# Kernel optimization log

Measured on AMD Instinct MI355X. Metric: run time of the kernel, lower is better.

## Reference

```python
import jax, jax.numpy as jnp
import numpy as np

B, IN_UNITS, IN_CH, NUM_UNITS, UNIT_SIZE = 32, 16, 2048, 16, 64
NUM_ITERS = 2


def setup_inputs() -> dict:
    key = jax.random.key(0)
    k1, k2 = jax.random.split(key)
    x = jax.random.normal(k1, (B, IN_UNITS, IN_CH), dtype=jnp.float32)
    W = jax.random.normal(k2, (1, IN_CH, NUM_UNITS, UNIT_SIZE, IN_UNITS), dtype=jnp.float32)
    return {"x": x, "W": W}


def squash(s):
    # torch code sums squared magnitude over dim=2 (the num_units axis) with keepdim
    mag_sq = jnp.sum(s * s, axis=2, keepdims=True)
    mag = jnp.sqrt(mag_sq)
    return mag_sq / (1.0 + mag_sq) * (s / mag)


def reference(x, W):
    # x: (B, in_units, in_channels) -> (B, in_channels, in_units)
    xt = jnp.swapaxes(x, 1, 2)
    # u_hat[b,i,j,k] = sum_u W[0,i,j,k,u] * xt[b,i,u]  -> (B, IC, NU, US)
    u_hat = jnp.einsum('ijku,biu->bijk', W[0], xt)
    b_ij = jnp.zeros((1, IN_CH, NUM_UNITS, 1), dtype=x.dtype)
    v_j = None
    for _ in range(NUM_ITERS):
        # softmax over a singleton trailing dim -> all ones (faithful to source)
        c_ij = jax.nn.softmax(b_ij, axis=-1)  # (1, IC, NU, 1), broadcasts over batch
        s_j = jnp.sum(c_ij[None, ..., 0][0][None].squeeze(0) * 0 + c_ij * u_hat, axis=1, keepdims=True) if False else jnp.sum(c_ij * u_hat, axis=1, keepdims=True)  # (B,1,NU,US)
        v_j = squash(s_j)  # (B,1,NU,US)
        # agreement: <u_hat, v_j> over unit_size, broadcast v_j over in_channels
        u_vj1 = jnp.einsum('bijk,bljk->bij', u_hat, v_j)  # (B, IC, NU)
        u_vj1 = jnp.mean(u_vj1, axis=0, keepdims=True)[..., None]  # (1, IC, NU, 1)
        b_ij = b_ij + u_vj1
    return v_j[:, 0, :, :]  # (B, num_units, unit_size)
```

## Files before the change

### kernel.cpp

```cpp
#include <hip/hip_runtime.h>
#include <hip/hip_bf16.h>


#define B_SZ   32
#define IC     2048
#define NJ     16
#define NK     64
#define SOUT   (B_SZ*NJ*NK)
#define KSTEPS 1024
#define KSPLIT 32
#define SPW    (KSTEPS/KSPLIT)

typedef float v4f __attribute__((ext_vector_type(4)));
typedef short v8s __attribute__((ext_vector_type(8)));

static __device__ inline ushort f2bf(float f) {
    uint32_t u = __float_as_uint(f);
    u += 0x7FFFu + ((u >> 16) & 1u);
    return (ushort)(u >> 16);
}

__global__ __launch_bounds__(256)
void caps_xprep(const float* __restrict__ x, ushort* __restrict__ xb) {
    int gid  = blockIdx.x * 256 + threadIdx.x;
    int lane = gid & 63;
    int mt   = (gid >> 6) & 1;
    int step = gid >> 7;
    int q    = lane >> 4;
    int b    = mt * 16 + (lane & 15);
    int i    = 2 * step + (q >> 1);
    int u0   = (q & 1) * 8;

    const float* xp = x + (size_t)b * (16 * IC) + (size_t)u0 * IC + i;
    ushort tmp[8];
    #pragma unroll
    for (int jj = 0; jj < 8; ++jj)
        tmp[jj] = f2bf(xp[(size_t)jj * IC]);
    *(v8s*)(xb + (size_t)gid * 8) = *(const v8s*)tmp;
}

__global__ __launch_bounds__(256)
void caps_mfma(const ushort* __restrict__ xb, const float* __restrict__ W,
               float* __restrict__ part) {
    const int tid   = threadIdx.x;
    const int wv    = tid >> 6;
    const int lane  = tid & 63;
    const int j     = blockIdx.x;
    const int split = blockIdx.y;
    const int n     = lane & 15;
    const int q     = lane >> 4;
    const int step0 = split * SPW;

    v4f acc0 = {0.f, 0.f, 0.f, 0.f};
    v4f acc1 = {0.f, 0.f, 0.f, 0.f};

    const float*  wp = W + (size_t)(2 * step0 + (q >> 1)) * 16384
                         + (size_t)j * 1024 + (size_t)(wv * 16 + n) * 16 + (q & 1) * 8;
    const ushort* xp = xb + (size_t)step0 * 1024 + (size_t)lane * 8;

    #pragma unroll 4
    for (int s = 0; s < SPW; ++s) {
        float4 w0 = *(const float4*)(wp);
        float4 w1 = *(const float4*)(wp + 4);
        v8s a0 = *(const v8s*)(xp);
        v8s a1 = *(const v8s*)(xp + 512);
        v8s bb;
        bb[0] = (short)f2bf(w0.x); bb[1] = (short)f2bf(w0.y);
        bb[2] = (short)f2bf(w0.z); bb[3] = (short)f2bf(w0.w);
        bb[4] = (short)f2bf(w1.x); bb[5] = (short)f2bf(w1.y);
        bb[6] = (short)f2bf(w1.z); bb[7] = (short)f2bf(w1.w);
        acc0 = __builtin_amdgcn_mfma_f32_16x16x32_bf16(a0, bb, acc0, 0, 0, 0);
        acc1 = __builtin_amdgcn_mfma_f32_16x16x32_bf16(a1, bb, acc1, 0, 0, 0);
        wp += 2 * 16384;
        xp += 1024;
    }

    float* pp = part + (size_t)split * SOUT + (size_t)j * NK + wv * 16 + n;
    #pragma unroll
    for (int r = 0; r < 4; ++r) {
        int m = q * 4 + r;
        pp[(size_t)m * 1024]        = acc0[r];
        pp[(size_t)(m + 16) * 1024] = acc1[r];
    }
}

__global__ __launch_bounds__(256)
void caps_finish(const float* __restrict__ part, float* __restrict__ out) {
    __shared__ float ls[256];
    const int blk = blockIdx.x;
    const int b   = blk >> 2;
    const int k0  = (blk & 3) * 16;
    const int t   = threadIdx.x;
    const int jj  = t >> 4;
    const int kc  = t & 15;
    const size_t idx = (size_t)b * 1024 + (size_t)jj * NK + k0 + kc;

    float s = 0.0f;
    #pragma unroll 8
    for (int sp = 0; sp < KSPLIT; ++sp)
        s += part[(size_t)sp * SOUT + idx];
    ls[t] = s;
    __syncthreads();

    float msq = 0.0f;
    #pragma unroll
    for (int j2 = 0; j2 < NJ; ++j2) {
        float v = ls[j2 * 16 + kc];
        msq += v * v;
    }
    float mag = sqrtf(msq);
    out[idx] = s * (mag / (1.0f + msq));
}

extern "C" void kernel_launch(void* const* d_in, const int* in_sizes, int n_in,
                              void* d_out, int out_size, void* d_ws, size_t ws_size,
                              hipStream_t stream) {
    const float* x = (const float*)d_in[0];
    const float* W = (const float*)d_in[1];
    float* out  = (float*)d_out;

    float*  part = (float*)d_ws;
    ushort* xb   = (ushort*)(part + (size_t)KSPLIT * SOUT);

    caps_xprep <<<512,               256, 0, stream>>>(x, xb);
    caps_mfma  <<<dim3(16, KSPLIT),  256, 0, stream>>>(xb, W, part);
    caps_finish<<<128,               256, 0, stream>>>(part, out);
}
```

Before: 201.9 us.

## Raise K-split, software-prefetch W/x loads, and cheapen bf16 packing

```diff
diff --git a/kernel.cpp b/kernel.cpp
--- a/kernel.cpp
+++ b/kernel.cpp
@@ -8,16 +8,23 @@
 #define NK     64
 #define SOUT   (B_SZ*NJ*NK)
 #define KSTEPS 1024
-#define KSPLIT 32
+#define KSPLIT 128
 #define SPW    (KSTEPS/KSPLIT)
 
 typedef float v4f __attribute__((ext_vector_type(4)));
 typedef short v8s __attribute__((ext_vector_type(8)));
+typedef unsigned int v4u __attribute__((ext_vector_type(4)));
 
 static __device__ inline ushort f2bf(float f) {
     uint32_t u = __float_as_uint(f);
     u += 0x7FFFu + ((u >> 16) & 1u);
     return (ushort)(u >> 16);
+}
+
+static __device__ inline uint packbf(float f0, float f1) {
+    uint u0 = __float_as_uint(f0) + 0x8000u;
+    uint u1 = __float_as_uint(f1) + 0x8000u;
+    return __builtin_amdgcn_perm(u1, u0, 0x07060302u);
 }
 
 __global__ __launch_bounds__(256)
@@ -39,7 +46,7 @@
     *(v8s*)(xb + (size_t)gid * 8) = *(const v8s*)tmp;
 }
 
-__global__ __launch_bounds__(256)
+__global__ __launch_bounds__(256, 6)
 void caps_mfma(const ushort* __restrict__ xb, const float* __restrict__ W,
                float* __restrict__ part) {
     const int tid   = threadIdx.x;
@@ -58,21 +65,36 @@
                          + (size_t)j * 1024 + (size_t)(wv * 16 + n) * 16 + (q & 1) * 8;
     const ushort* xp = xb + (size_t)step0 * 1024 + (size_t)lane * 8;
 
-    #pragma unroll 4
-    for (int s = 0; s < SPW; ++s) {
-        float4 w0 = *(const float4*)(wp);
-        float4 w1 = *(const float4*)(wp + 4);
-        v8s a0 = *(const v8s*)(xp);
-        v8s a1 = *(const v8s*)(xp + 512);
-        v8s bb;
-        bb[0] = (short)f2bf(w0.x); bb[1] = (short)f2bf(w0.y);
-        bb[2] = (short)f2bf(w0.z); bb[3] = (short)f2bf(w0.w);
-        bb[4] = (short)f2bf(w1.x); bb[5] = (short)f2bf(w1.y);
-        bb[6] = (short)f2bf(w1.z); bb[7] = (short)f2bf(w1.w);
+    float4 w0 = *(const float4*)(wp);
+    float4 w1 = *(const float4*)(wp + 4);
+    v8s    a0 = *(const v8s*)(xp);
+    v8s    a1 = *(const v8s*)(xp + 512);
+
+    #pragma unroll
+    for (int s = 0; s < SPW - 1; ++s) {
+        wp += 2 * 16384;
+        xp += 1024;
+        float4 nw0 = *(const float4*)(wp);
+        float4 nw1 = *(const float4*)(wp + 4);
+        v8s    na0 = *(const v8s*)(xp);
+        v8s    na1 = *(const v8s*)(xp + 512);
+
+        v4u pk;
+        pk.x = packbf(w0.x, w0.y); pk.y = packbf(w0.z, w0.w);
+        pk.z = packbf(w1.x, w1.y); pk.w = packbf(w1.z, w1.w);
+        v8s bb = *(v8s*)&pk;
         acc0 = __builtin_amdgcn_mfma_f32_16x16x32_bf16(a0, bb, acc0, 0, 0, 0);
         acc1 = __builtin_amdgcn_mfma_f32_16x16x32_bf16(a1, bb, acc1, 0, 0, 0);
-        wp += 2 * 16384;
-        xp += 1024;
+
+        w0 = nw0; w1 = nw1; a0 = na0; a1 = na1;
+    }
+    {
+        v4u pk;
+        pk.x = packbf(w0.x, w0.y); pk.y = packbf(w0.z, w0.w);
+        pk.z = packbf(w1.x, w1.y); pk.w = packbf(w1.z, w1.w);
+        v8s bb = *(v8s*)&pk;
+        acc0 = __builtin_amdgcn_mfma_f32_16x16x32_bf16(a0, bb, acc0, 0, 0, 0);
+        acc1 = __builtin_amdgcn_mfma_f32_16x16x32_bf16(a1, bb, acc1, 0, 0, 0);
     }
 
     float* pp = part + (size_t)split * SOUT + (size_t)j * NK + wv * 16 + n;
```

Result: slower. 208.4 us (+3.2%).
